# Optimization experiments

Measured on AMD Instinct MI355X. Metric: run time of the kernel, lower is better.

## Reference

```python
import jax, jax.numpy as jnp
import numpy as np

B, S = 2048, 16384
DELAY = 5.0  # self._delay


def setup_inputs() -> dict:
    key = jax.random.key(0)
    k1, k2, k3 = jax.random.split(key, 3)
    logits = jax.random.normal(k1, (B, S, 1), dtype=jnp.float32)
    # ragged valid lengths; positions >= length are zero-padded (what the
    # torch while-loop trims as trailing zeros)
    lengths = jax.random.randint(k2, (B,), S // 4, S, dtype=jnp.int32)
    pad_mask = jnp.arange(S)[None, :] < lengths[:, None]  # [B,S]
    logits = logits * pad_mask[:, :, None].astype(jnp.float32)
    target = jax.random.uniform(k3, (B, 1), dtype=jnp.float32)
    return {"input": logits, "lengths": lengths, "target": target}


def reference(input, lengths, target):
    # input: [B,S,1] zero-padded logits; target: [B,1]
    x = input[..., 0]  # [B,S]
    seq = x.shape[1]
    # Replicate the torch trimming: last = -1; while pred[last]==0: last-=1;
    # pred = pred[:last] keeps exactly `idx` elements where idx is the index
    # of the last nonzero entry.
    nz = x != 0.0
    idx = seq - 1 - jnp.argmax(nz[:, ::-1], axis=1)  # [B], kept length L_i
    pos = jnp.arange(seq)
    keep = (pos[None, :] < idx[:, None]).astype(x.dtype)  # [B,S]
    # BCEWithLogits, reduction='none', default weights
    t = target  # [B,1] broadcasts over S
    bce = jnp.maximum(x, 0.0) - x * t + jnp.log1p(jnp.exp(-jnp.abs(x)))
    # position-dependent confidence weight: sigmoid(j - delay), masked to kept region
    w = jax.nn.sigmoid(pos.astype(x.dtype) - DELAY)[None, :] * keep  # [B,S]
    per_sample = (bce * w).sum(axis=1) / w.sum(axis=1)  # [B]
    return per_sample.mean()
```

## Files before the change

kernel.cpp:

```cpp
#include <hip/hip_runtime.h>
#include <math.h>


#define LN2F 0.69314718055994531f

__device__ __forceinline__ float bce_nat(float x, float t) {
    const float e = __expf(-fabsf(x));
    return fmaf(-x, t, fmaxf(x, 0.0f) + __logf(1.0f + e));
}

#define ACC(xv) do {                                   \
    const float e_ = __expf(-fabsf(xv));               \
    Alog += __log2f(1.0f + e_);                        \
    Alin += fmaf(-(xv), t, fmaxf((xv), 0.0f)); } while (0)

__global__ __launch_bounds__(256) void half_row_kernel(
    const float* __restrict__ x, const int* __restrict__ lengths,
    const float* __restrict__ target, float4* __restrict__ pA,
    float4* __restrict__ pB, int S)
{
    const int bid = blockIdx.x;
    const int b = bid >> 1;
    const bool isB = (bid & 1) != 0;
    const float* row = x + (size_t)b * (size_t)S;
    const float t = target[b];
    const int tid = threadIdx.x;
    const int len = min(max(lengths[b], 1), S);
    const int L4 = (len + 3) & ~3;
    const int H  = (L4 >> 3) << 2;
    const int lo = isB ? H : 0;
    const int hi = isB ? L4 : H;
    const int n  = hi - lo;
    const int lastb = lo + (((n - 1) >> 12) << 12);

    __shared__ float s_head[24];
    __shared__ float sLin[4], sLog[4], sV[4];
    __shared__ int   sI[4];
    __shared__ float s_lin, s_log;

    if (!isB && tid < 6)
        *reinterpret_cast<float4*>(&s_head[tid * 4]) =
            *reinterpret_cast<const float4*>(row + tid * 4);

    float Alin = 0.0f, Alog = 0.0f;
    int maxidx = -1; float mval = 0.0f;

    for (int base = lo; base < lastb; base += 4096) {
        const int j0 = base + tid * 4;
        const float4 v0 = *reinterpret_cast<const float4*>(row + j0);
        const float4 v1 = *reinterpret_cast<const float4*>(row + j0 + 1024);
        const float4 v2 = *reinterpret_cast<const float4*>(row + j0 + 2048);
        const float4 v3 = *reinterpret_cast<const float4*>(row + j0 + 3072);
        const float vs[16] = {v0.x, v0.y, v0.z, v0.w, v1.x, v1.y, v1.z, v1.w,
                              v2.x, v2.y, v2.z, v2.w, v3.x, v3.y, v3.z, v3.w};
        #pragma unroll
        for (int k = 0; k < 16; ++k) { const float xv = vs[k]; ACC(xv); }
    }

    if (isB) {
        #pragma unroll
        for (int seg = 0; seg < 4; ++seg) {
            const int j0 = lastb + (seg << 10) + tid * 4;
            if (j0 < hi) {
                const float4 v = *reinterpret_cast<const float4*>(row + j0);
                const float vs[4] = {v.x, v.y, v.z, v.w};
                #pragma unroll
                for (int k = 0; k < 4; ++k) {
                    const float xv = vs[k]; ACC(xv);
                    if (xv != 0.0f) { maxidx = j0 + k; mval = xv; }
                }
            }
        }
    } else {
        #pragma unroll
        for (int seg = 0; seg < 4; ++seg) {
            const int j0 = lastb + (seg << 10) + tid * 4;
            if (j0 < hi) {
                const float4 v = *reinterpret_cast<const float4*>(row + j0);
                const float vs[4] = {v.x, v.y, v.z, v.w};
                #pragma unroll
                for (int k = 0; k < 4; ++k) { const float xv = vs[k]; ACC(xv); }
            }
        }
    }

    #pragma unroll
    for (int off = 32; off > 0; off >>= 1) {
        Alin += __shfl_down(Alin, off);
        Alog += __shfl_down(Alog, off);
        const int   oi = __shfl_down(maxidx, off);
        const float ov = __shfl_down(mval, off);
        if (oi > maxidx) { maxidx = oi; mval = ov; }
    }
    const int wave = tid >> 6;
    if ((tid & 63) == 0) { sLin[wave] = Alin; sLog[wave] = Alog;
                           sI[wave] = maxidx; sV[wave] = mval; }
    __syncthreads();

    if (isB) {
        if (tid == 0) {
            #pragma unroll
            for (int w = 1; w < 4; ++w) {
                Alin += sLin[w]; Alog += sLog[w];
                if (sI[w] > maxidx) { maxidx = sI[w]; mval = sV[w]; }
            }
            const int idx = (maxidx < 0) ? (hi - 1) : maxidx;
            pB[b] = make_float4(Alin, Alog, __int_as_float(idx), mval);
        }
    } else {
        if (tid == 0) {
            #pragma unroll
            for (int w = 1; w < 4; ++w) { Alin += sLin[w]; Alog += sLog[w]; }
            s_lin = Alin; s_log = Alog;
        }
        __syncthreads();
        if (tid < 64) {
            float c = 0.0f, d = 0.0f;
            if (tid < 22) {
                const float sg = 1.0f / (1.0f + __expf(5.0f - (float)tid));
                c = bce_nat(s_head[tid], t) * (sg - 1.0f);
                d = sg;
            }
            #pragma unroll
            for (int off = 32; off > 0; off >>= 1) {
                c += __shfl_down(c, off);
                d += __shfl_down(d, off);
            }
            if (tid == 0)
                pA[b] = make_float4(s_lin + c, s_log, d, 0.0f);
        }
    }
}

__global__ __launch_bounds__(1024) void combine_kernel(
    const float4* __restrict__ pA, const float4* __restrict__ pB,
    const int* __restrict__ lengths, const float* __restrict__ target,
    float* __restrict__ out, int S, int B)
{
    const int tid = threadIdx.x;
    float s = 0.0f;
    for (int r = tid; r < B; r += 1024) {
        const float4 a  = pA[r];
        const float4 bq = pB[r];
        const float  t  = target[r];
        const int len = min(max(lengths[r], 1), S);
        const int L4  = (len + 3) & ~3;
        const int idx = __float_as_int(bq.z);
        const float mval = bq.w;
        const float e_m  = __expf(-fabsf(mval));
        const float Alog = a.y + bq.y - __log2f(1.0f + e_m)
                           - (float)(L4 - 1 - idx);
        const float Alin = a.x + bq.x - fmaf(-mval, t, fmaxf(mval, 0.0f));
        const float den  = a.z + (float)(idx - 22);
        s += (Alin + LN2F * Alog) / den;
    }
    #pragma unroll
    for (int off = 32; off > 0; off >>= 1) s += __shfl_down(s, off);
    __shared__ float sw[16];
    if ((tid & 63) == 0) sw[tid >> 6] = s;
    __syncthreads();
    if (tid == 0) {
        float tot = 0.0f;
        #pragma unroll
        for (int w = 0; w < 16; ++w) tot += sw[w];
        out[0] = tot / (float)B;
    }
}

extern "C" void kernel_launch(void* const* d_in, const int* in_sizes, int n_in,
                              void* d_out, int out_size, void* d_ws, size_t ws_size,
                              hipStream_t stream) {
    const float* logits  = (const float*)d_in[0];
    const int*   lengths = (const int*)d_in[1];
    const float* target  = (const float*)d_in[2];
    float* out = (float*)d_out;

    const int B = in_sizes[2];
    const int S = in_sizes[0] / B;

    float4* pA = (float4*)d_ws;
    float4* pB = pA + B;

    half_row_kernel<<<2 * B, 256, 0, stream>>>(logits, lengths, target,
                                               pA, pB, S);
    combine_kernel<<<1, 1024, 0, stream>>>(pA, pB, lengths, target, out, S, B);
}
```

Measured before the change: 23.49 us.

## Split rows into fixed 4096-element segment blocks and use a log of products

Replaces the two-blocks-per-row split with four blocks per row, one per fixed 4096-element segment. Blocks whose segment lies entirely past the valid length exit early, and only the boundary segment tracks the last nonzero element. The per-element log2(1+e) is replaced by a running product of (1+e) in four independent accumulators, with a single log2 taken at the end, which removes most transcendental work. The combine kernel now sums per-segment partials. The block index decoding assumes exactly four segments per row, and the product form adds some overflow and precision risk.

```diff
diff --git a/kernel.cpp b/kernel.cpp
--- a/kernel.cpp
+++ b/kernel.cpp
@@ -9,80 +9,89 @@
     return fmaf(-x, t, fmaxf(x, 0.0f) + __logf(1.0f + e));
 }
 
-#define ACC(xv) do {                                   \
-    const float e_ = __expf(-fabsf(xv));               \
-    Alog += __log2f(1.0f + e_);                        \
-    Alin += fmaf(-(xv), t, fmaxf((xv), 0.0f)); } while (0)
-
-__global__ __launch_bounds__(256) void half_row_kernel(
+__global__ __launch_bounds__(256) void seg_kernel(
     const float* __restrict__ x, const int* __restrict__ lengths,
-    const float* __restrict__ target, float4* __restrict__ pA,
-    float4* __restrict__ pB, int S)
+    const float* __restrict__ target, float4* __restrict__ pseg,
+    float2* __restrict__ phead, int S)
 {
     const int bid = blockIdx.x;
-    const int b = bid >> 1;
-    const bool isB = (bid & 1) != 0;
+    const int b = bid >> 2;
+    const int s = bid & 3;
+    const int tid = threadIdx.x;
+
+    const int len = min(max(lengths[b], 1), S);
+    const int L4  = (len + 3) & ~3;
+    const int lo  = s << 12;
+    if (lo >= L4) return;
+
+    const int s_last = (L4 - 1) >> 12;
+    const bool boundary = (s == s_last);
     const float* row = x + (size_t)b * (size_t)S;
     const float t = target[b];
-    const int tid = threadIdx.x;
-    const int len = min(max(lengths[b], 1), S);
-    const int L4 = (len + 3) & ~3;
-    const int H  = (L4 >> 3) << 2;
-    const int lo = isB ? H : 0;
-    const int hi = isB ? L4 : H;
-    const int n  = hi - lo;
-    const int lastb = lo + (((n - 1) >> 12) << 12);
 
     __shared__ float s_head[24];
     __shared__ float sLin[4], sLog[4], sV[4];
     __shared__ int   sI[4];
-    __shared__ float s_lin, s_log;
 
-    if (!isB && tid < 6)
+    if (s == 0 && tid < 6)
         *reinterpret_cast<float4*>(&s_head[tid * 4]) =
             *reinterpret_cast<const float4*>(row + tid * 4);
 
-    float Alin = 0.0f, Alog = 0.0f;
+    float P0 = 1.0f, P1 = 1.0f, P2 = 1.0f, P3 = 1.0f;
+    float A0 = 0.0f, A1 = 0.0f, A2 = 0.0f, A3 = 0.0f;
     int maxidx = -1; float mval = 0.0f;
 
-    for (int base = lo; base < lastb; base += 4096) {
-        const int j0 = base + tid * 4;
+    const int j0 = lo + tid * 4;
+
+#define GRP(vv, jj, PP, AA) do {                                   \
+    const float g_[4] = {vv.x, vv.y, vv.z, vv.w};                  \
+    _Pragma("unroll")                                              \
+    for (int k_ = 0; k_ < 4; ++k_) {                               \
+        const float xv_ = g_[k_];                                  \
+        PP *= 1.0f + __expf(-fabsf(xv_));                          \
+        AA += fmaf(-xv_, t, fmaxf(xv_, 0.0f));                     \
+    } } while (0)
+
+#define GRPI(vv, jj, PP, AA) do {                                  \
+    const float g_[4] = {vv.x, vv.y, vv.z, vv.w};                  \
+    _Pragma("unroll")                                              \
+    for (int k_ = 0; k_ < 4; ++k_) {                               \
+        const float xv_ = g_[k_];                                  \
+        PP *= 1.0f + __expf(-fabsf(xv_));                          \
+        AA += fmaf(-xv_, t, fmaxf(xv_, 0.0f));                     \
+        if (xv_ != 0.0f) { maxidx = (jj) + k_; mval = xv_; }       \
+    } } while (0)
+
+    if (!boundary) {
         const float4 v0 = *reinterpret_cast<const float4*>(row + j0);
         const float4 v1 = *reinterpret_cast<const float4*>(row + j0 + 1024);
         const float4 v2 = *reinterpret_cast<const float4*>(row + j0 + 2048);
         const float4 v3 = *reinterpret_cast<const float4*>(row + j0 + 3072);
-        const float vs[16] = {v0.x, v0.y, v0.z, v0.w, v1.x, v1.y, v1.z, v1.w,
-                              v2.x, v2.y, v2.z, v2.w, v3.x, v3.y, v3.z, v3.w};
-        #pragma unroll
-        for (int k = 0; k < 16; ++k) { const float xv = vs[k]; ACC(xv); }
+        GRP(v0, j0,        P0, A0);
+        GRP(v1, j0 + 1024, P1, A1);
+        GRP(v2, j0 + 2048, P2, A2);
+        GRP(v3, j0 + 3072, P3, A3);
+    } else {
+        if (j0 < L4) {
+            const float4 v = *reinterpret_cast<const float4*>(row + j0);
+            GRPI(v, j0, P0, A0);
+        }
+        if (j0 + 1024 < L4) {
+            const float4 v = *reinterpret_cast<const float4*>(row + j0 + 1024);
+            GRPI(v, j0 + 1024, P1, A1);
+        }
+        if (j0 + 2048 < L4) {
+            const float4 v = *reinterpret_cast<const float4*>(row + j0 + 2048);
+            GRPI(v, j0 + 2048, P2, A2);
+        }
+        if (j0 + 3072 < L4) {
+            const float4 v = *reinterpret_cast<const float4*>(row + j0 + 3072);
+            GRPI(v, j0 + 3072, P3, A3);
+        }
     }
 
-    if (isB) {
-        #pragma unroll
-        for (int seg = 0; seg < 4; ++seg) {
-            const int j0 = lastb + (seg << 10) + tid * 4;
-            if (j0 < hi) {
-                const float4 v = *reinterpret_cast<const float4*>(row + j0);
-                const float vs[4] = {v.x, v.y, v.z, v.w};
-                #pragma unroll
-                for (int k = 0; k < 4; ++k) {
-                    const float xv = vs[k]; ACC(xv);
-                    if (xv != 0.0f) { maxidx = j0 + k; mval = xv; }
-                }
-            }
-        }
-    } else {
-        #pragma unroll
-        for (int seg = 0; seg < 4; ++seg) {
-            const int j0 = lastb + (seg << 10) + tid * 4;
-            if (j0 < hi) {
-                const float4 v = *reinterpret_cast<const float4*>(row + j0);
-                const float vs[4] = {v.x, v.y, v.z, v.w};
-                #pragma unroll
-                for (int k = 0; k < 4; ++k) { const float xv = vs[k]; ACC(xv); }
-            }
-        }
-    }
+    float Alin = (A0 + A1) + (A2 + A3);
+    float Alog = __log2f(((P0 * P1) * (P2 * P3)));
 
     #pragma unroll
     for (int off = 32; off > 0; off >>= 1) {
@@ -97,22 +106,17 @@
                            sI[wave] = maxidx; sV[wave] = mval; }
     __syncthreads();
 
-    if (isB) {
-        if (tid == 0) {
-            #pragma unroll
-            for (int w = 1; w < 4; ++w) {
-                Alin += sLin[w]; Alog += sLog[w];
-                if (sI[w] > maxidx) { maxidx = sI[w]; mval = sV[w]; }
-            }
-            const int idx = (maxidx < 0) ? (hi - 1) : maxidx;
-            pB[b] = make_float4(Alin, Alog, __int_as_float(idx), mval);
+    if (tid == 0) {
+        #pragma unroll
+        for (int w = 1; w < 4; ++w) {
+            Alin += sLin[w]; Alog += sLog[w];
+            if (sI[w] > maxidx) { maxidx = sI[w]; mval = sV[w]; }
         }
-    } else {
-        if (tid == 0) {
-            #pragma unroll
-            for (int w = 1; w < 4; ++w) { Alin += sLin[w]; Alog += sLog[w]; }
-            s_lin = Alin; s_log = Alog;
-        }
+        if (boundary && maxidx < 0) { maxidx = L4 - 1; mval = 0.0f; }
+        pseg[bid] = make_float4(Alin, Alog, __int_as_float(maxidx), mval);
+    }
+
+    if (s == 0) {
         __syncthreads();
         if (tid < 64) {
             float c = 0.0f, d = 0.0f;
@@ -126,38 +130,42 @@
                 c += __shfl_down(c, off);
                 d += __shfl_down(d, off);
             }
-            if (tid == 0)
-                pA[b] = make_float4(s_lin + c, s_log, d, 0.0f);
+            if (tid == 0) phead[b] = make_float2(c, d);
         }
     }
 }
 
 __global__ __launch_bounds__(1024) void combine_kernel(
-    const float4* __restrict__ pA, const float4* __restrict__ pB,
+    const float4* __restrict__ pseg, const float2* __restrict__ phead,
     const int* __restrict__ lengths, const float* __restrict__ target,
     float* __restrict__ out, int S, int B)
 {
     const int tid = threadIdx.x;
-    float s = 0.0f;
+    float acc = 0.0f;
     for (int r = tid; r < B; r += 1024) {
-        const float4 a  = pA[r];
-        const float4 bq = pB[r];
-        const float  t  = target[r];
         const int len = min(max(lengths[r], 1), S);
         const int L4  = (len + 3) & ~3;
-        const int idx = __float_as_int(bq.z);
-        const float mval = bq.w;
+        const int s_last = (L4 - 1) >> 12;
+        float Alin = 0.0f, Alog = 0.0f;
+        float4 q;
+        for (int s = 0; s <= s_last; ++s) {
+            q = pseg[(r << 2) + s];
+            Alin += q.x; Alog += q.y;
+        }
+        const int   idx  = __float_as_int(q.z);
+        const float mval = q.w;
+        const float t    = target[r];
+        const float2 hd  = phead[r];
         const float e_m  = __expf(-fabsf(mval));
-        const float Alog = a.y + bq.y - __log2f(1.0f + e_m)
-                           - (float)(L4 - 1 - idx);
-        const float Alin = a.x + bq.x - fmaf(-mval, t, fmaxf(mval, 0.0f));
-        const float den  = a.z + (float)(idx - 22);
-        s += (Alin + LN2F * Alog) / den;
+        Alog -= __log2f(1.0f + e_m) + (float)(L4 - 1 - idx);
+        Alin -= fmaf(-mval, t, fmaxf(mval, 0.0f));
+        const float den = hd.y + (float)(idx - 22);
+        acc += (Alin + hd.x + LN2F * Alog) / den;
     }
     #pragma unroll
-    for (int off = 32; off > 0; off >>= 1) s += __shfl_down(s, off);
+    for (int off = 32; off > 0; off >>= 1) acc += __shfl_down(acc, off);
     __shared__ float sw[16];
-    if ((tid & 63) == 0) sw[tid >> 6] = s;
+    if ((tid & 63) == 0) sw[tid >> 6] = acc;
     __syncthreads();
     if (tid == 0) {
         float tot = 0.0f;
@@ -177,11 +185,13 @@
 
     const int B = in_sizes[2];
     const int S = in_sizes[0] / B;
+    const int NSEG = S >> 12;
 
-    float4* pA = (float4*)d_ws;
-    float4* pB = pA + B;
+    float4* pseg  = (float4*)d_ws;
+    float2* phead = (float2*)(pseg + (size_t)B * NSEG);
 
-    half_row_kernel<<<2 * B, 256, 0, stream>>>(logits, lengths, target,
-                                               pA, pB, S);
-    combine_kernel<<<1, 1024, 0, stream>>>(pA, pB, lengths, target, out, S, B);
+    seg_kernel<<<B * NSEG, 256, 0, stream>>>(logits, lengths, target,
+                                             pseg, phead, S);
+    combine_kernel<<<1, 1024, 0, stream>>>(pseg, phead, lengths, target,
+                                           out, S, B);
 }
```

New measurement: 27.06 us. +15.2%, slower.
